# Performance work log

Measured on AMD Instinct MI355X. Metric: run time of the kernel, lower is better.

The kernel has to match this reference:

```python
import jax, jax.numpy as jnp
import numpy as np

N = 500_000   # num nodes
F = 128       # num_features
H = 128       # hidden
B = 32_768    # batch size
K = 4         # hops
RWS = 16      # random walks per batch node
E = RWS * B   # sampled edges per hop
ALPHA = 0.1
OUT = 8


def setup_inputs() -> dict:
    key = jax.random.key(0)
    ks = jax.random.split(key, 12)
    x = jax.random.normal(ks[0], (N, F), dtype=jnp.float32)
    degree = jax.random.uniform(ks[1], (N,), dtype=jnp.float32, minval=1.0, maxval=64.0)
    batch = jax.random.randint(ks[2], (B,), 0, N, dtype=jnp.int32)
    heads_idx = jax.random.randint(ks[3], (K, E), 0, B, dtype=jnp.int32)
    ends = jax.random.randint(ks[4], (K, E), 0, N, dtype=jnp.int32)
    # MLP params (Kaiming-ish scaling)
    W0 = jax.random.normal(ks[5], (F, H), dtype=jnp.float32) / np.float32(np.sqrt(F))
    b0 = jnp.zeros((H,), dtype=jnp.float32)
    W1 = jax.random.normal(ks[6], (H, H), dtype=jnp.float32) / np.float32(np.sqrt(H))
    b1 = jnp.zeros((H,), dtype=jnp.float32)
    W2 = jax.random.normal(ks[7], (H, OUT), dtype=jnp.float32) / np.float32(np.sqrt(H))
    b2 = jnp.zeros((OUT,), dtype=jnp.float32)
    # APPNP attention weights: alpha*(1-alpha)^k, last = (1-alpha)^K
    att = np.float32(ALPHA) * np.float32(1.0 - ALPHA) ** np.arange(K + 1, dtype=np.float32)
    att[-1] = np.float32(1.0 - ALPHA) ** np.float32(K)
    att = jnp.asarray(att)
    return {"x": x, "W0": W0, "b0": b0, "W1": W1, "b1": b1, "W2": W2, "b2": b2,
            "att": att, "degree": degree, "batch": batch,
            "heads_idx": heads_idx, "ends": ends}


def reference(x, W0, b0, W1, b1, W2, b2, att, degree, batch, heads_idx, ends):
    # eval mode: dropout is a no-op
    dis = degree ** -0.5  # deg_inv_sqrt

    def mlp(feats):  # lins[1](relu(lins[0](feats)))
        h = jax.nn.relu(feats @ W0 + b0)
        return h @ W1 + b1

    nb = batch.shape[0]
    ne = jnp.float32(ends.shape[1])
    dsum = degree[batch].sum()

    aggx = att[0] * mlp(x[batch])                       # [B, H]
    for k in range(K):  # small fixed hop count
        heads = heads_idx[k]                            # local rows in [0, B)
        e = ends[k]                                     # global node ids
        val = dis[batch[heads]] * dis[e] * (dsum / ne)  # [E]
        tmp = mlp(x[e]) * val[:, None]                  # gather + MLP + weight
        aggx = aggx + att[k + 1] * jax.ops.segment_sum(tmp, heads, num_segments=nb)
    out = jax.nn.relu(aggx) @ W2 + b2                   # [B, 8]
    return jax.nn.log_softmax(out, axis=1)
```

## Files before the change

kernel.cpp:

```cpp
#include <hip/hip_runtime.h>

#define NN 500000
#define FF 128
#define HH 128
#define BB 32768
#define KHOPS 4
#define EPER 524288
#define KE (KHOPS * EPER)
#define NOUT 8
#define SBLK 256
#define EPB (KE / SBLK)
#define GEMM_TILES 3907

typedef unsigned short u16;
typedef unsigned char u8;
typedef __attribute__((ext_vector_type(8))) short short8v;
typedef __attribute__((ext_vector_type(4))) float f32x4;
typedef __attribute__((ext_vector_type(2))) float f32x2;

__device__ __forceinline__ float bflo(unsigned int u) {
    union { unsigned int x; float f; } t; t.x = u << 16; return t.f;
}
__device__ __forceinline__ float bfhi(unsigned int u) {
    union { unsigned int x; float f; } t; t.x = u & 0xFFFF0000u; return t.f;
}
__device__ __forceinline__ u16 f2bf(float f) {
    union { float f; unsigned int u; } t; t.f = f;
    unsigned int u = t.u;
    unsigned int r = (u + 0x7FFFu + ((u >> 16) & 1u)) >> 16;
    return (u16)r;
}

__launch_bounds__(256, 2)
__global__ void k_pre1(const int* __restrict__ heads, u8* __restrict__ M,
                       const float* __restrict__ deg, const int* __restrict__ batch,
                       float* __restrict__ dsum, const float* __restrict__ W0,
                       u16* __restrict__ w0p, float* __restrict__ dis) {
    __shared__ unsigned int hp[8192];
    int tid = threadIdx.x;
    int bid = blockIdx.x;
    if (bid < SBLK) {
        #pragma unroll
        for (int j = 0; j < 32; j++) hp[tid + j * 256] = 0;
        __syncthreads();
        int ebase = bid * EPB;
        #pragma unroll 4
        for (int it = 0; it < EPB / 256; it++) {
            int b = heads[ebase + it * 256 + tid];
            atomicAdd(&hp[b >> 2], 1u << ((b & 3) * 8));
        }
        __syncthreads();
        unsigned int* M32 = (unsigned int*)(M + (size_t)bid * BB);
        #pragma unroll
        for (int j = 0; j < 32; j++) {
            int w = tid + j * 256;
            M32[w] = hp[w];
        }
    } else if (bid == SBLK) {
        float* red = (float*)hp;
        float a0 = 0.f, a1 = 0.f, a2 = 0.f, a3 = 0.f;
        for (int i = tid; i < BB; i += 1024) {
            a0 += deg[batch[i]];
            a1 += deg[batch[i + 256]];
            a2 += deg[batch[i + 512]];
            a3 += deg[batch[i + 768]];
        }
        red[tid] = (a0 + a1) + (a2 + a3);
        __syncthreads();
        for (int off = 128; off > 0; off >>= 1) {
            if (tid < off) red[tid] += red[tid + off];
            __syncthreads();
        }
        if (tid == 0) dsum[0] = red[0];
    } else if (bid == SBLK + 1) {
        for (int r = 0; r < 64; r++) {
            int f = r * 256 + tid;
            int k = f >> 7, c = f & 127;
            int kt = k >> 5, i = k & 7, lh = (k >> 3) & 3;
            int lane = lh * 16 + (c & 15), n = c >> 4;
            w0p[(((kt * 8 + n) * 64 + lane) << 3) + i] = f2bf(W0[f]);
        }
    } else {
        int i0 = (bid - SBLK - 2) * 1024 + tid * 4;
        if (i0 < NN) {
            float4 d = *(const float4*)&deg[i0];
            float4 o;
            o.x = rsqrtf(d.x); o.y = rsqrtf(d.y);
            o.z = rsqrtf(d.z); o.w = rsqrtf(d.w);
            *(float4*)&dis[i0] = o;
        }
    }
}

__global__ void k_pre2(u8* __restrict__ M, int* __restrict__ colsum,
                       const float* __restrict__ deg, const int* __restrict__ batch,
                       const float* __restrict__ dsum, float* __restrict__ disb) {
    int tid = threadIdx.x;
    if (blockIdx.x < 32) {
        int g = blockIdx.x * 256 + tid;
        unsigned int* M32 = (unsigned int*)M;
        unsigned int run = 0;
        #pragma unroll 8
        for (int b = 0; b < SBLK; b++) {
            size_t idx = (size_t)b * (BB / 4) + g;
            unsigned int v = M32[idx];
            M32[idx] = run;
            run += v;
        }
        colsum[g * 4 + 0] = (int)(run & 0xFFu);
        colsum[g * 4 + 1] = (int)((run >> 8) & 0xFFu);
        colsum[g * 4 + 2] = (int)((run >> 16) & 0xFFu);
        colsum[g * 4 + 3] = (int)((run >> 24) & 0xFFu);
    } else {
        int b0 = (blockIdx.x - 32) * 1024 + tid * 4;
        float sc = dsum[0] * (1.0f / (float)EPER);
        #pragma unroll
        for (int t = 0; t < 4; t++) {
            int b = b0 + t;
            disb[b] = rsqrtf(deg[batch[b]]) * sc;
        }
    }
}

__global__ void k_scan(const int* __restrict__ colsum, int* __restrict__ base) {
    __shared__ int sc[1024];
    int tid = threadIdx.x;
    int loc[32];
    int run = 0;
    #pragma unroll
    for (int j = 0; j < 32; j++) {
        loc[j] = run;
        run += colsum[tid * 32 + j];
    }
    sc[tid] = run;
    __syncthreads();
    for (int off = 1; off < 1024; off <<= 1) {
        int v = (tid >= off) ? sc[tid - off] : 0;
        __syncthreads();
        sc[tid] += v;
        __syncthreads();
    }
    int excl = sc[tid] - run;
    #pragma unroll
    for (int j = 0; j < 32; j++) base[tid * 32 + j] = excl + loc[j];
    if (tid == 1023) base[BB] = sc[1023];
}

__launch_bounds__(256, 2)
__global__ void k_fused(const float* __restrict__ x, const u16* __restrict__ w0p,
                        const float* __restrict__ b0, u16* __restrict__ h,
                        const int* __restrict__ heads, const int* __restrict__ ends,
                        const u8* __restrict__ M, const int* __restrict__ base,
                        const float* __restrict__ dis, const float* __restrict__ disb,
                        const float* __restrict__ att, uint2* __restrict__ ewp) {
    __shared__ char smem[65536];
    int tid = threadIdx.x;

    if (blockIdx.x < SBLK) {
        unsigned int* hp = (unsigned int*)smem;
        int blk = blockIdx.x;
        float attk = att[(blk >> 6) + 1];
        #pragma unroll
        for (int j = 0; j < 32; j++) hp[tid + j * 256] = 0;
        __syncthreads();
        int ebase = blk * EPB;
        for (int it = 0; it < EPB / 256; it++) {
            int i = ebase + it * 256 + tid;
            int b = heads[i];
            int e = ends[i];
            float w = attk * disb[b] * dis[e];
            unsigned int old = atomicAdd(&hp[b >> 2], 1u << ((b & 3) * 8));
            unsigned int rank = (old >> ((b & 3) * 8)) & 0xFFu;
            int pos = base[b] + (int)M[(size_t)blk * BB + b] + (int)rank;
            uint2 pw;
            pw.x = (unsigned int)e;
            pw.y = __float_as_uint(w);
            ewp[pos] = pw;
        }
        return;
    }

    u16* xs = (u16*)smem;
    u16* ws = (u16*)(smem + 32768);
    int wid = tid >> 6;
    int lane = tid & 63;
    long rowbase = (long)(blockIdx.x - SBLK) * 128;

    #pragma unroll
    for (int r = 0; r < 8; r++) {
        int f = tid + r * 256;
        *(float4*)&ws[f * 8] = *(const float4*)&w0p[f * 8];
    }
    #pragma unroll
    for (int r = 0; r < 16; r++) {
        int f = tid + r * 256;
        int row = f >> 5;
        int c4 = (f & 31) * 4;
        long grow = rowbase + row; if (grow >= NN) grow = NN - 1;
        float4 v = *(const float4*)&x[grow * 128 + c4];
        ushort4 pv;
        pv.x = f2bf(v.x); pv.y = f2bf(v.y); pv.z = f2bf(v.z); pv.w = f2bf(v.w);
        int byte = row * 256 + ((c4 * 2) ^ ((row & 7) << 4));
        *(ushort4*)((char*)xs + byte) = pv;
    }
    __syncthreads();

    short8v a[2][4];
    #pragma unroll
    for (int rs = 0; rs < 2; rs++) {
        int row = wid * 32 + rs * 16 + (lane & 15);
        int sw = (row & 7) << 4;
        #pragma unroll
        for (int kt = 0; kt < 4; kt++) {
            int kb = kt * 64 + (lane >> 4) * 16;
            a[rs][kt] = *(const short8v*)((const char*)xs + row * 256 + (kb ^ sw));
        }
    }

    f32x4 acc[2][8] = {};
    #pragma unroll
    for (int n = 0; n < 8; n++) {
        short8v bfr[4];
        #pragma unroll
        for (int kt = 0; kt < 4; kt++)
            bfr[kt] = *(const short8v*)&ws[(((kt * 8 + n) * 64 + lane) << 3)];
        #pragma unroll
        for (int rs = 0; rs < 2; rs++) {
            #pragma unroll
            for (int kt = 0; kt < 4; kt++)
                acc[rs][n] = __builtin_amdgcn_mfma_f32_16x16x32_bf16(
                                 a[rs][kt], bfr[kt], acc[rs][n], 0, 0, 0);
        }
    }

    float b0v[8];
    #pragma unroll
    for (int n = 0; n < 8; n++) b0v[n] = b0[n * 16 + (lane & 15)];

    u16* xw = &xs[wid * 32 * 128];
    #pragma unroll
    for (int rs = 0; rs < 2; rs++) {
        #pragma unroll
        for (int r = 0; r < 4; r++) {
            int row = rs * 16 + (lane >> 4) * 4 + r;
            int sw = (row & 7) << 4;
            #pragma unroll
            for (int n = 0; n < 8; n++) {
                float v = acc[rs][n][r] + b0v[n];
                v = v > 0.f ? v : 0.f;
                int byte = row * 256 + ((n * 32 + (lane & 15) * 2) ^ sw);
                *(u16*)((char*)xw + byte) = f2bf(v);
            }
        }
    }
    __syncthreads();
    #pragma unroll
    for (int pass = 0; pass < 8; pass++) {
        int off = pass * 1024 + lane * 16;
        int row = off >> 8;
        int colb = off & 255;
        int ocolb = colb ^ ((row & 7) << 4);
        long grow = rowbase + wid * 32 + row;
        uint4 v = *(const uint4*)((const char*)xw + off);
        if (grow < NN)
            *(uint4*)((char*)&h[grow * 128] + ocolb) = v;
    }
}

__launch_bounds__(256)
__global__ void k_gather(const u16* __restrict__ h, const int* __restrict__ batch,
                         const int* __restrict__ base, const uint2* __restrict__ ewp,
                         const float* __restrict__ att,
                         float* __restrict__ P, float* __restrict__ s) {
    int b = blockIdx.x * 4 + (threadIdx.x >> 6);
    int l = threadIdx.x & 63;
    int q = l >> 4;
    int c8 = (l & 15) * 8;
    float att0 = att[0];
    f32x2 acc2[4] = {{0.f, 0.f}, {0.f, 0.f}, {0.f, 0.f}, {0.f, 0.f}};
    float wsum = 0.f;

    if (q == 0) {
        int nb = batch[b];
        uint4 v = *(const uint4*)&h[(size_t)nb * 128 + c8];
        acc2[0] = f32x2{att0 * bflo(v.x), att0 * bfhi(v.x)};
        acc2[1] = f32x2{att0 * bflo(v.y), att0 * bfhi(v.y)};
        acc2[2] = f32x2{att0 * bflo(v.z), att0 * bfhi(v.z)};
        acc2[3] = f32x2{att0 * bflo(v.w), att0 * bfhi(v.w)};
    }

    int beg = base[b], fin = base[b + 1];
    for (int j = beg; j < fin; j += 32) {
        uint2 pw[8];
        #pragma unroll
        for (int u = 0; u < 8; u++) {
            int je = j + u * 4 + q;
            int jc = je < fin ? je : beg;
            pw[u] = ewp[jc];
            if (je >= fin) pw[u].y = 0u;
        }
        uint4 v[8];
        #pragma unroll
        for (int u = 0; u < 8; u++)
            v[u] = *(const uint4*)&h[(size_t)pw[u].x * 128 + c8];
        #pragma unroll
        for (int u = 0; u < 8; u++) {
            float w = __uint_as_float(pw[u].y);
            f32x2 w2 = {w, w};
            acc2[0] = __builtin_elementwise_fma(w2, f32x2{bflo(v[u].x), bfhi(v[u].x)}, acc2[0]);
            acc2[1] = __builtin_elementwise_fma(w2, f32x2{bflo(v[u].y), bfhi(v[u].y)}, acc2[1]);
            acc2[2] = __builtin_elementwise_fma(w2, f32x2{bflo(v[u].z), bfhi(v[u].z)}, acc2[2]);
            acc2[3] = __builtin_elementwise_fma(w2, f32x2{bflo(v[u].w), bfhi(v[u].w)}, acc2[3]);
            wsum += w;
        }
    }
    float accf[8] = { acc2[0].x, acc2[0].y, acc2[1].x, acc2[1].y,
                      acc2[2].x, acc2[2].y, acc2[3].x, acc2[3].y };
    #pragma unroll
    for (int k = 0; k < 8; k++) {
        accf[k] += __shfl_xor(accf[k], 16);
        accf[k] += __shfl_xor(accf[k], 32);
    }
    wsum += __shfl_xor(wsum, 16);
    wsum += __shfl_xor(wsum, 32);

    if (q == 0) {
        float4 o0 = { accf[0], accf[1], accf[2], accf[3] };
        float4 o1 = { accf[4], accf[5], accf[6], accf[7] };
        *(float4*)&P[(size_t)b * 128 + c8]     = o0;
        *(float4*)&P[(size_t)b * 128 + c8 + 4] = o1;
        if (l == 0) s[b] = att0 + wsum;
    }
}

__launch_bounds__(256, 2)
__global__ void k_out(const float* __restrict__ P, const float* __restrict__ s,
                      const float* __restrict__ W1, const float* __restrict__ b1,
                      const float* __restrict__ W2, const float* __restrict__ b2,
                      float* __restrict__ out) {
    __shared__ float W1s[128 * 128];
    __shared__ float Ps[32 * 128];
    int tid = threadIdx.x;
    int rowbase = blockIdx.x * 32;
    #pragma unroll
    for (int rep = 0; rep < 16; rep++) {
        int f = tid + rep * 256;
        *(float4*)&W1s[f * 4] = *(const float4*)&W1[f * 4];
    }
    #pragma unroll
    for (int rep = 0; rep < 4; rep++) {
        int f = tid + rep * 256;
        *(float4*)&Ps[f * 4] = *(const float4*)&P[(size_t)rowbase * 128 + f * 4];
    }
    __syncthreads();

    int c0 = (tid & 31) * 4;
    int r0 = (tid >> 5) * 4;
    float b1r[4] = { b1[c0], b1[c0 + 1], b1[c0 + 2], b1[c0 + 3] };
    float sv[4];
    #pragma unroll
    for (int j = 0; j < 4; j++) sv[j] = s[rowbase + r0 + j];

    float acc[4][4] = {};
    #pragma unroll 2
    for (int i = 0; i < 128; i += 4) {
        float4 xq[4], wq4[4];
        #pragma unroll
        for (int j = 0; j < 4; j++) xq[j]  = *(const float4*)&Ps[(r0 + j) * 128 + i];
        #pragma unroll
        for (int q = 0; q < 4; q++) wq4[q] = *(const float4*)&W1s[(i + q) * 128 + c0];
        #pragma unroll
        for (int j = 0; j < 4; j++) {
            float xv[4] = { xq[j].x, xq[j].y, xq[j].z, xq[j].w };
            #pragma unroll
            for (int q = 0; q < 4; q++) {
                acc[j][0] += xv[q] * wq4[q].x;
                acc[j][1] += xv[q] * wq4[q].y;
                acc[j][2] += xv[q] * wq4[q].z;
                acc[j][3] += xv[q] * wq4[q].w;
            }
        }
    }
    __syncthreads();
    #pragma unroll
    for (int j = 0; j < 4; j++) {
        #pragma unroll
        for (int c = 0; c < 4; c++) {
            float v = acc[j][c] + sv[j] * b1r[c];
            Ps[(r0 + j) * 128 + c0 + c] = v > 0.f ? v : 0.f;
        }
    }
    __syncthreads();

    int row = tid >> 3;
    int o = tid & 7;
    int rot = (row * 4) & 127;
    float v = b2[o];
    #pragma unroll 4
    for (int ii = 0; ii < 128; ii++) {
        int i = (ii + rot) & 127;
        v += Ps[row * 128 + i] * W2[i * 8 + o];
    }
    float m = v;
    for (int d = 1; d < 8; d <<= 1) m = fmaxf(m, __shfl_xor(m, d, 8));
    float ex = expf(v - m);
    float sum = ex;
    for (int d = 1; d < 8; d <<= 1) sum += __shfl_xor(sum, d, 8);
    out[(size_t)(rowbase + row) * 8 + o] = (v - m) - logf(sum);
}

extern "C" void kernel_launch(void* const* d_in, const int* in_sizes, int n_in,
                              void* d_out, int out_size, void* d_ws, size_t ws_size,
                              hipStream_t stream) {
    const float* x     = (const float*)d_in[0];
    const float* W0    = (const float*)d_in[1];
    const float* b0    = (const float*)d_in[2];
    const float* W1    = (const float*)d_in[3];
    const float* b1    = (const float*)d_in[4];
    const float* W2    = (const float*)d_in[5];
    const float* b2    = (const float*)d_in[6];
    const float* att   = (const float*)d_in[7];
    const float* deg   = (const float*)d_in[8];
    const int*   batch = (const int*)d_in[9];
    const int*   heads = (const int*)d_in[10];
    const int*   ends  = (const int*)d_in[11];
    float* out = (float*)d_out;

    char* w = (char*)d_ws;
    size_t off = 0;
    u16* h = (u16*)(w + off);          off += (size_t)NN * 128 * 2;
    float* P = (float*)(w + off);      off += (size_t)BB * 128 * 4;
    float* s = (float*)(w + off);      off += (size_t)BB * 4;
    int* base = (int*)(w + off);       off += 131328;
    uint2* ewp = (uint2*)(w + off);    off += (size_t)KE * 8;
    u8* M = (u8*)(w + off);            off += (size_t)SBLK * BB;
    int* colsum = (int*)(w + off);     off += (size_t)BB * 4;
    float* dis = (float*)(w + off);    off += (size_t)NN * 4;
    float* disb = (float*)(w + off);   off += (size_t)BB * 4;
    float* dsum = (float*)(w + off);   off += 256;
    u16* w0p = (u16*)(w + off);        off += 16384 * 2;

    int disBlocks = (NN + 1023) / 1024;
    k_pre1<<<SBLK + 2 + disBlocks, 256, 0, stream>>>(heads, M, deg, batch,
                                                     dsum, W0, w0p, dis);
    k_pre2<<<64, 256, 0, stream>>>(M, colsum, deg, batch, dsum, disb);
    k_scan<<<1, 1024, 0, stream>>>(colsum, base);
    k_fused<<<SBLK + GEMM_TILES, 256, 0, stream>>>(x, w0p, b0, h, heads, ends,
                                                   M, base, dis, disb, att, ewp);
    k_gather<<<BB / 4, 256, 0, stream>>>(h, batch, base, ewp, att, P, s);
    k_out<<<BB / 32, 256, 0, stream>>>(P, s, W1, b1, W2, b2, out);
}
```

Measured before the change: 347.9 us.

## Split fused scatter/GEMM kernel and read W0 fragments directly from global

Splits the combined scatter-plus-GEMM kernel into a dedicated edge scatter kernel and a standalone first-layer GEMM kernel. The GEMM kernel drops its W0 shared-memory staging and loads B fragments straight from global memory, which halves LDS use per block and raises launch bounds for higher occupancy. In exchange, the scatter and GEMM no longer overlap within one launch and run back to back on the same stream, and W0 is reread from global or cache for every tile.

```diff
diff --git a/kernel.cpp b/kernel.cpp
--- a/kernel.cpp
+++ b/kernel.cpp
@@ -147,50 +147,41 @@
 }
 
 __launch_bounds__(256, 2)
-__global__ void k_fused(const float* __restrict__ x, const u16* __restrict__ w0p,
-                        const float* __restrict__ b0, u16* __restrict__ h,
-                        const int* __restrict__ heads, const int* __restrict__ ends,
-                        const u8* __restrict__ M, const int* __restrict__ base,
-                        const float* __restrict__ dis, const float* __restrict__ disb,
-                        const float* __restrict__ att, uint2* __restrict__ ewp) {
-    __shared__ char smem[65536];
+__global__ void k_scatter2(const int* __restrict__ heads, const int* __restrict__ ends,
+                           const u8* __restrict__ M, const int* __restrict__ base,
+                           const float* __restrict__ dis, const float* __restrict__ disb,
+                           const float* __restrict__ att, uint2* __restrict__ ewp) {
+    __shared__ unsigned int hp[8192];
+    int tid = threadIdx.x, blk = blockIdx.x;
+    float attk = att[(blk >> 6) + 1];
+    #pragma unroll
+    for (int j = 0; j < 32; j++) hp[tid + j * 256] = 0;
+    __syncthreads();
+    int ebase = blk * EPB;
+    for (int it = 0; it < EPB / 256; it++) {
+        int i = ebase + it * 256 + tid;
+        int b = heads[i];
+        int e = ends[i];
+        float w = attk * disb[b] * dis[e];
+        unsigned int old = atomicAdd(&hp[b >> 2], 1u << ((b & 3) * 8));
+        unsigned int rank = (old >> ((b & 3) * 8)) & 0xFFu;
+        int pos = base[b] + (int)M[(size_t)blk * BB + b] + (int)rank;
+        uint2 pw;
+        pw.x = (unsigned int)e;
+        pw.y = __float_as_uint(w);
+        ewp[pos] = pw;
+    }
+}
+
+__launch_bounds__(256, 5)
+__global__ void k_gemm1(const float* __restrict__ x, const u16* __restrict__ w0p,
+                        const float* __restrict__ b0, u16* __restrict__ h) {
+    __shared__ u16 xs[128 * 128];
     int tid = threadIdx.x;
-
-    if (blockIdx.x < SBLK) {
-        unsigned int* hp = (unsigned int*)smem;
-        int blk = blockIdx.x;
-        float attk = att[(blk >> 6) + 1];
-        #pragma unroll
-        for (int j = 0; j < 32; j++) hp[tid + j * 256] = 0;
-        __syncthreads();
-        int ebase = blk * EPB;
-        for (int it = 0; it < EPB / 256; it++) {
-            int i = ebase + it * 256 + tid;
-            int b = heads[i];
-            int e = ends[i];
-            float w = attk * disb[b] * dis[e];
-            unsigned int old = atomicAdd(&hp[b >> 2], 1u << ((b & 3) * 8));
-            unsigned int rank = (old >> ((b & 3) * 8)) & 0xFFu;
-            int pos = base[b] + (int)M[(size_t)blk * BB + b] + (int)rank;
-            uint2 pw;
-            pw.x = (unsigned int)e;
-            pw.y = __float_as_uint(w);
-            ewp[pos] = pw;
-        }
-        return;
-    }
-
-    u16* xs = (u16*)smem;
-    u16* ws = (u16*)(smem + 32768);
     int wid = tid >> 6;
     int lane = tid & 63;
-    long rowbase = (long)(blockIdx.x - SBLK) * 128;
-
-    #pragma unroll
-    for (int r = 0; r < 8; r++) {
-        int f = tid + r * 256;
-        *(float4*)&ws[f * 8] = *(const float4*)&w0p[f * 8];
-    }
+    long rowbase = (long)blockIdx.x * 128;
+
     #pragma unroll
     for (int r = 0; r < 16; r++) {
         int f = tid + r * 256;
@@ -223,7 +214,7 @@
         short8v bfr[4];
         #pragma unroll
         for (int kt = 0; kt < 4; kt++)
-            bfr[kt] = *(const short8v*)&ws[(((kt * 8 + n) * 64 + lane) << 3)];
+            bfr[kt] = *(const short8v*)&w0p[(((kt * 8 + n) * 64 + lane) << 3)];
         #pragma unroll
         for (int rs = 0; rs < 2; rs++) {
             #pragma unroll
@@ -445,8 +436,8 @@
                                                      dsum, W0, w0p, dis);
     k_pre2<<<64, 256, 0, stream>>>(M, colsum, deg, batch, dsum, disb);
     k_scan<<<1, 1024, 0, stream>>>(colsum, base);
-    k_fused<<<SBLK + GEMM_TILES, 256, 0, stream>>>(x, w0p, b0, h, heads, ends,
-                                                   M, base, dis, disb, att, ewp);
+    k_scatter2<<<SBLK, 256, 0, stream>>>(heads, ends, M, base, dis, disb, att, ewp);
+    k_gemm1<<<GEMM_TILES, 256, 0, stream>>>(x, w0p, b0, h);
     k_gather<<<BB / 4, 256, 0, stream>>>(h, batch, base, ewp, att, P, s);
     k_out<<<BB / 32, 256, 0, stream>>>(P, s, W1, b1, W2, b2, out);
 }
```

New measurement: 370.9 us. 1.07x slower.
